# Optimization experiments

Hardware: AMD Instinct MI355X
Metric: run time of the kernel (lower is better)

Reference implementation:

```python
import jax, jax.numpy as jnp
import numpy as np

N = 50000      # number of atoms/nodes
D = 32         # atom_dim == units (pad_length = 0)
E = 300000     # number of bonds/edges
BD = 16        # bond_dim
STEPS = 4      # message passing steps


def setup_inputs() -> dict:
    key = jax.random.key(0)
    ks = jax.random.split(key, 8)
    atom_features = jax.random.normal(ks[0], (N, D), dtype=jnp.float32)
    bond_features = jax.random.uniform(ks[1], (E, BD), dtype=jnp.float32)
    pair_indices = jax.random.randint(ks[2], (E, 2), 0, N, dtype=jnp.int32)
    # EdgeNetwork kernel: xavier_uniform on [bond_dim, atom_dim*atom_dim]
    s = float(np.sqrt(6.0 / (BD + D * D)))
    kernel = jax.random.uniform(ks[3], (BD, D * D), dtype=jnp.float32, minval=-s, maxval=s)
    bias = jnp.zeros((D * D,), dtype=jnp.float32)
    # torch.nn.GRUCell init: U(-1/sqrt(H), 1/sqrt(H)), H = D (pad_length = 0)
    stdv = float(1.0 / np.sqrt(D))
    W_ih = jax.random.uniform(ks[4], (3 * D, D), dtype=jnp.float32, minval=-stdv, maxval=stdv)
    W_hh = jax.random.uniform(ks[5], (3 * D, D), dtype=jnp.float32, minval=-stdv, maxval=stdv)
    b_ih = jax.random.uniform(ks[6], (3 * D,), dtype=jnp.float32, minval=-stdv, maxval=stdv)
    b_hh = jax.random.uniform(ks[7], (3 * D,), dtype=jnp.float32, minval=-stdv, maxval=stdv)
    return {
        "atom_features": atom_features,
        "bond_features": bond_features,
        "pair_indices": pair_indices,
        "kernel": kernel,
        "bias": bias,
        "W_ih": W_ih,
        "W_hh": W_hh,
        "b_ih": b_ih,
        "b_hh": b_hh,
    }


def _gru_cell(x, h, W_ih, W_hh, b_ih, b_hh):
    # torch.nn.GRUCell math, gates stacked as (r, z, n)
    gi = x @ W_ih.T + b_ih  # [N, 3D]
    gh = h @ W_hh.T + b_hh  # [N, 3D]
    i_r, i_z, i_n = jnp.split(gi, 3, axis=-1)
    h_r, h_z, h_n = jnp.split(gh, 3, axis=-1)
    r = jax.nn.sigmoid(i_r + h_r)
    z = jax.nn.sigmoid(i_z + h_z)
    n = jnp.tanh(i_n + r * h_n)
    return (1.0 - z) * n + z * h


def reference(atom_features, bond_features, pair_indices, kernel, bias, W_ih, W_hh, b_ih, b_hh):
    # pad_length = units - atom_dim = 0, so no padding needed.
    W = kernel.reshape(BD, D, D)   # per-bond-feature DxD transforms
    Bm = bias.reshape(D, D)        # bias as DxD matrix applied to neighbor feats
    dst = pair_indices[:, 0]       # aggregation (index_add) target
    src = pair_indices[:, 1]       # gathered neighbor

    h = atom_features
    for _ in range(STEPS):
        nbr = h[src]  # [E, D] gather
        # transformed[e, i] = sum_j (bond[e] @ kernel + bias)[i, j] * nbr[e, j]
        msg = jnp.einsum('eb,bij,ej->ei', bond_features, W, nbr) + nbr @ Bm.T
        agg = jax.ops.segment_sum(msg, dst, num_segments=N)  # scatter-add
        h = _gru_cell(agg, h, W_ih, W_hh, b_ih, b_hh)
    return h
```

## Files before the change

### kernel.cpp

```cpp
#include <hip/hip_runtime.h>
#include <math.h>

#define N_ATOMS 50000
#define D 32
#define E_EDGES 300000
#define BD 16
#define SW 544
#define SCAN_BLOCKS ((N_ATOMS + 255) / 256)
#define GRU_TILE 8
#define GRU_NT (N_ATOMS / GRU_TILE)

#define NB 32
#define FBLOCKS ((N_ATOMS + NB - 1) / NB)

__device__ __forceinline__ float sigmoidf_(float x) {
    return 1.0f / (1.0f + __expf(-x));
}


__global__ void k_build_wt(const float* __restrict__ kern,
                           const float* __restrict__ bias,
                           float* __restrict__ WTj) {
    int idx = blockIdx.x * 256 + threadIdx.x;
    if (idx >= 32 * SW) return;
    int j = idx / SW;
    int r = idx - j * SW;
    int b = r >> 5, i = r & 31;
    WTj[idx] = (b < BD) ? kern[b * 1024 + i * 32 + j] : bias[i * 32 + j];
}

__global__ void k_hist(const int* __restrict__ pair, int* __restrict__ deg, int col) {
    int e = blockIdx.x * 256 + threadIdx.x;
    if (e < E_EDGES) atomicAdd(&deg[pair[2 * e + col]], 1);
}

__global__ void k_scan1(const int* __restrict__ deg, int* __restrict__ offs,
                        int* __restrict__ bsums) {
    __shared__ int sm[256];
    int t = threadIdx.x, gid = blockIdx.x * 256 + t;
    int v = (gid < N_ATOMS) ? deg[gid] : 0;
    sm[t] = v;
    __syncthreads();
    for (int off = 1; off < 256; off <<= 1) {
        int x = (t >= off) ? sm[t - off] : 0;
        __syncthreads();
        sm[t] += x;
        __syncthreads();
    }
    if (gid < N_ATOMS) offs[gid] = sm[t] - v;
    if (t == 255) bsums[blockIdx.x] = sm[255];
}

__global__ void k_scan2(const int* __restrict__ bsums, int* __restrict__ boffs, int nb) {
    __shared__ int sm[256];
    int t = threadIdx.x;
    int v = (t < nb) ? bsums[t] : 0;
    sm[t] = v;
    __syncthreads();
    for (int off = 1; off < 256; off <<= 1) {
        int x = (t >= off) ? sm[t - off] : 0;
        __syncthreads();
        sm[t] += x;
        __syncthreads();
    }
    if (t < nb) boffs[t] = sm[t] - v;
}

__global__ void k_scan3(int* __restrict__ offs, const int* __restrict__ boffs) {
    int gid = blockIdx.x * 256 + threadIdx.x;
    if (gid < N_ATOMS) offs[gid] += boffs[blockIdx.x];
}

__global__ void k_scatter_perm(const int* __restrict__ pair, const int* __restrict__ offs,
                               int* __restrict__ cursor, const float* __restrict__ bond,
                               float* __restrict__ bond_perm, int* __restrict__ dstid) {
    int e = blockIdx.x * 256 + threadIdx.x;
    if (e >= E_EDGES) return;
    int d = pair[2 * e], s = pair[2 * e + 1];
    int pos = offs[s] + atomicAdd(&cursor[s], 1);
    dstid[pos] = d;
    const float4* src4 = (const float4*)(bond + (size_t)e * BD);
    float4* dst4 = (float4*)(bond_perm + (size_t)pos * BD);
    dst4[0] = src4[0];
    dst4[1] = src4[1];
    dst4[2] = src4[2];
    dst4[3] = src4[3];
}

__global__ void k_dstpos(const int* __restrict__ dstid, const int* __restrict__ offs2,
                         int* __restrict__ cursor2, int* __restrict__ wpos) {
    int p = blockIdx.x * 256 + threadIdx.x;
    if (p >= E_EDGES) return;
    int d = dstid[p];
    wpos[p] = offs2[d] + atomicAdd(&cursor2[d], 1);
}

#define EDGE_FMA(M, B0, B1, B2, B3, YN) do {            \
    M = fmaf(B0.x, YN[0],  M); M = fmaf(B0.y, YN[1],  M); \
    M = fmaf(B0.z, YN[2],  M); M = fmaf(B0.w, YN[3],  M); \
    M = fmaf(B1.x, YN[4],  M); M = fmaf(B1.y, YN[5],  M); \
    M = fmaf(B1.z, YN[6],  M); M = fmaf(B1.w, YN[7],  M); \
    M = fmaf(B2.x, YN[8],  M); M = fmaf(B2.y, YN[9],  M); \
    M = fmaf(B2.z, YN[10], M); M = fmaf(B2.w, YN[11], M); \
    M = fmaf(B3.x, YN[12], M); M = fmaf(B3.y, YN[13], M); \
    M = fmaf(B3.z, YN[14], M); M = fmaf(B3.w, YN[15], M); \
} while (0)

__global__ __launch_bounds__(256, 2)
void k_msg(const float* __restrict__ h_in, float* __restrict__ msg_d,
           const float* __restrict__ bond_perm, const int* __restrict__ wpos,
           const float* __restrict__ WTj,
           const int* __restrict__ offs, const int* __restrict__ deg) {
    __shared__ float h_lds[NB][33];

    const int t = threadIdx.x;
    const int bbase = blockIdx.x * NB;
    const int i = t & 31;
    const int grp = t >> 5;
    const int hn0 = grp * 4;

#pragma unroll
    for (int k = 0; k < 4; ++k) {
        const int idx = t + 256 * k;
        const int n = idx >> 5, j = idx & 31;
        const int node = bbase + n;
        h_lds[n][j] = (node < N_ATOMS) ? h_in[(size_t)node * D + j] : 0.f;
    }

    int stv[4], env[4];
#pragma unroll
    for (int n = 0; n < 4; ++n) {
        const int node = bbase + hn0 + n;
        const bool ok = (node < N_ATOMS);
        const int o = ok ? offs[node] : 0;
        stv[n] = o;
        env[n] = o + (ok ? deg[node] : 0);
    }
    __syncthreads();

    float y[4][17];
#pragma unroll
    for (int n = 0; n < 4; ++n)
#pragma unroll
        for (int b = 0; b < 17; ++b) y[n][b] = 0.f;

    for (int j = 0; j < 32; ++j) {
        float wv[17];
#pragma unroll
        for (int b = 0; b < 17; ++b)
            wv[b] = WTj[j * SW + b * 32 + i];
#pragma unroll
        for (int n = 0; n < 4; ++n) {
            const float hv = h_lds[hn0 + n][j];
#pragma unroll
            for (int b = 0; b < 17; ++b)
                y[n][b] = fmaf(wv[b], hv, y[n][b]);
        }
    }

#pragma unroll
    for (int n = 0; n < 4; ++n) {
        int p = stv[n];
        const int e = env[n];
        for (; p + 2 <= e; p += 2) {
            const float4* bp0 = (const float4*)(bond_perm + (size_t)p * BD);
            const float4* bp1 = (const float4*)(bond_perm + (size_t)(p + 1) * BD);
            const int w0 = wpos[p];
            const int w1 = wpos[p + 1];
            const float4 a0 = bp0[0], a1 = bp0[1], a2 = bp0[2], a3 = bp0[3];
            const float4 c0 = bp1[0], c1 = bp1[1], c2 = bp1[2], c3 = bp1[3];
            float m0 = y[n][16];
            float m1 = y[n][16];
            EDGE_FMA(m0, a0, a1, a2, a3, y[n]);
            EDGE_FMA(m1, c0, c1, c2, c3, y[n]);
            msg_d[(size_t)w0 * D + i] = m0;
            msg_d[(size_t)w1 * D + i] = m1;
        }
        if (p < e) {
            const float4* bp0 = (const float4*)(bond_perm + (size_t)p * BD);
            const int w0 = wpos[p];
            const float4 a0 = bp0[0], a1 = bp0[1], a2 = bp0[2], a3 = bp0[3];
            float m0 = y[n][16];
            EDGE_FMA(m0, a0, a1, a2, a3, y[n]);
            msg_d[(size_t)w0 * D + i] = m0;
        }
    }
}

__global__ __launch_bounds__(256, 2)
void k_aggru(const float* __restrict__ msg_d,
             const int* __restrict__ offs2, const int* __restrict__ deg2,
             const float* __restrict__ h_in, float* __restrict__ h_out,
             const float* __restrict__ Wih, const float* __restrict__ Whh,
             const float* __restrict__ bih, const float* __restrict__ bhh) {
    __shared__ float Wih_s[96][33];
    __shared__ float Whh_s[96][33];
    __shared__ float bih_s[96], bhh_s[96];
    __shared__ float x_lds[GRU_TILE][32];
    __shared__ float h_lds[GRU_TILE][32];

    const int t = threadIdx.x;

    for (int idx = t; idx < 96 * 32; idx += 256) {
        const int o = idx >> 5, jj = idx & 31;
        Wih_s[o][jj] = Wih[idx];
        Whh_s[o][jj] = Whh[idx];
    }
    if (t < 96) { bih_s[t] = bih[t]; bhh_s[t] = bhh[t]; }

    const int r = t >> 5;
    const int i = t & 31;
    const int stride = gridDim.x;

    for (int tile = blockIdx.x; tile < GRU_NT; tile += stride) {
        const int node = tile * GRU_TILE + r;
        const int st = offs2[node];
        const int en = st + deg2[node];
        float acc = 0.f;
        int p = st;
        for (; p + 4 <= en; p += 4) {
            const float a0 = msg_d[(size_t)(p + 0) * D + i];
            const float a1 = msg_d[(size_t)(p + 1) * D + i];
            const float a2 = msg_d[(size_t)(p + 2) * D + i];
            const float a3 = msg_d[(size_t)(p + 3) * D + i];
            acc += (a0 + a1) + (a2 + a3);
        }
        for (; p < en; ++p) acc += msg_d[(size_t)p * D + i];
        x_lds[r][i] = acc;
        ((float*)h_lds)[t] = h_in[tile * 256 + t];
        __syncthreads();

        float gri = bih_s[i],      grh = bhh_s[i];
        float gzi = bih_s[32 + i], gzh = bhh_s[32 + i];
        float gni = bih_s[64 + i], gnh = bhh_s[64 + i];
#pragma unroll 8
        for (int jj = 0; jj < 32; ++jj) {
            const float xv = x_lds[r][jj];
            const float hv = h_lds[r][jj];
            gri = fmaf(Wih_s[i][jj],      xv, gri);
            gzi = fmaf(Wih_s[32 + i][jj], xv, gzi);
            gni = fmaf(Wih_s[64 + i][jj], xv, gni);
            grh = fmaf(Whh_s[i][jj],      hv, grh);
            gzh = fmaf(Whh_s[32 + i][jj], hv, gzh);
            gnh = fmaf(Whh_s[64 + i][jj], hv, gnh);
        }
        const float rg = sigmoidf_(gri + grh);
        const float zg = sigmoidf_(gzi + gzh);
        float xn = gni + rg * gnh;
        xn = fminf(fmaxf(xn, -15.f), 15.f);
        const float e2 = __expf(2.f * xn);
        const float ng = (e2 - 1.f) / (e2 + 1.f);
        h_out[tile * 256 + t] = (1.f - zg) * ng + zg * h_lds[r][i];
        __syncthreads();
    }
}

extern "C" void kernel_launch(void* const* d_in, const int* in_sizes, int n_in,
                              void* d_out, int out_size, void* d_ws, size_t ws_size,
                              hipStream_t stream) {
    const float* atom = (const float*)d_in[0];
    const float* bond = (const float*)d_in[1];
    const int*   pair = (const int*)d_in[2];
    const float* kern = (const float*)d_in[3];
    const float* bias = (const float*)d_in[4];
    const float* Wih  = (const float*)d_in[5];
    const float* Whh  = (const float*)d_in[6];
    const float* bih  = (const float*)d_in[7];
    const float* bhh  = (const float*)d_in[8];
    float* out = (float*)d_out;

    char* w = (char*)d_ws;
    auto alloc = [&](size_t bytes) {
        char* p = w;
        w += (bytes + 255) & ~size_t(255);
        return p;
    };
    float* hA        = (float*)alloc((size_t)N_ATOMS * D * 4);
    float* WTj       = (float*)alloc((size_t)32 * SW * 4);
    int*   deg       = (int*)alloc((size_t)N_ATOMS * 4);
    int*   offs      = (int*)alloc((size_t)N_ATOMS * 4);
    int*   deg2      = (int*)alloc((size_t)N_ATOMS * 4);
    int*   offs2     = (int*)alloc((size_t)N_ATOMS * 4);
    int*   cursor    = (int*)alloc((size_t)N_ATOMS * 4);
    int*   cursor2   = (int*)alloc((size_t)N_ATOMS * 4);
    int*   bsums     = (int*)alloc(256 * 4);
    int*   boffs     = (int*)alloc(256 * 4);
    int*   dstid     = (int*)alloc((size_t)E_EDGES * 4);
    int*   wpos      = (int*)alloc((size_t)E_EDGES * 4);
    float* bond_perm = (float*)alloc((size_t)E_EDGES * BD * 4);
    float* msg_d     = (float*)alloc((size_t)E_EDGES * D * 4);

    hipMemsetAsync(deg, 0, (size_t)N_ATOMS * 4, stream);
    hipMemsetAsync(deg2, 0, (size_t)N_ATOMS * 4, stream);
    hipMemsetAsync(cursor, 0, (size_t)N_ATOMS * 4, stream);
    hipMemsetAsync(cursor2, 0, (size_t)N_ATOMS * 4, stream);

    k_build_wt<<<(32 * SW + 255) / 256, 256, 0, stream>>>(kern, bias, WTj);
    k_hist<<<(E_EDGES + 255) / 256, 256, 0, stream>>>(pair, deg, 1);
    k_scan1<<<SCAN_BLOCKS, 256, 0, stream>>>(deg, offs, bsums);
    k_scan2<<<1, 256, 0, stream>>>(bsums, boffs, SCAN_BLOCKS);
    k_scan3<<<SCAN_BLOCKS, 256, 0, stream>>>(offs, boffs);
    k_hist<<<(E_EDGES + 255) / 256, 256, 0, stream>>>(pair, deg2, 0);
    k_scan1<<<SCAN_BLOCKS, 256, 0, stream>>>(deg2, offs2, bsums);
    k_scan2<<<1, 256, 0, stream>>>(bsums, boffs, SCAN_BLOCKS);
    k_scan3<<<SCAN_BLOCKS, 256, 0, stream>>>(offs2, boffs);
    k_scatter_perm<<<(E_EDGES + 255) / 256, 256, 0, stream>>>(pair, offs, cursor,
                                                              bond, bond_perm, dstid);
    k_dstpos<<<(E_EDGES + 255) / 256, 256, 0, stream>>>(dstid, offs2, cursor2, wpos);

    const float* hsrc = atom;
    float* hdst[4] = { hA, out, hA, out };
    for (int s = 0; s < 4; ++s) {
        k_msg<<<FBLOCKS, 256, 0, stream>>>(hsrc, msg_d, bond_perm, wpos,
                                           WTj, offs, deg);
        k_aggru<<<2048, 256, 0, stream>>>(msg_d, offs2, deg2, hsrc, hdst[s],
                                          Wih, Whh, bih, bhh);
        hsrc = hdst[s];
    }
}
```

Baseline: 564.2 us.

## Write messages contiguously in source order and gather them by index in aggregation

The message kernel now writes each edge's message at its source-sorted position instead of scattering it to the destination-sorted slot. The aggregation kernel reads it back through a new reverse-position index. This turns scattered writes into coalesced ones at the cost of indirect gathered reads plus an extra index load per edge. The message kernel also doubles its nodes per block from 32 to 64 (8 per warp group). That reuses each weight load across more nodes but raises register pressure, since y grows to 8x17 floats.

```diff
diff --git a/kernel.cpp b/kernel.cpp
--- a/kernel.cpp
+++ b/kernel.cpp
@@ -10,7 +10,7 @@
 #define GRU_TILE 8
 #define GRU_NT (N_ATOMS / GRU_TILE)
 
-#define NB 32
+#define NB 64
 #define FBLOCKS ((N_ATOMS + NB - 1) / NB)
 
 __device__ __forceinline__ float sigmoidf_(float x) {
@@ -87,12 +87,13 @@
     dst4[3] = src4[3];
 }
 
-__global__ void k_dstpos(const int* __restrict__ dstid, const int* __restrict__ offs2,
-                         int* __restrict__ cursor2, int* __restrict__ wpos) {
+__global__ void k_rpos(const int* __restrict__ dstid, const int* __restrict__ offs2,
+                       int* __restrict__ cursor2, int* __restrict__ rpos) {
     int p = blockIdx.x * 256 + threadIdx.x;
     if (p >= E_EDGES) return;
     int d = dstid[p];
-    wpos[p] = offs2[d] + atomicAdd(&cursor2[d], 1);
+    int slot = offs2[d] + atomicAdd(&cursor2[d], 1);
+    rpos[slot] = p;
 }
 
 #define EDGE_FMA(M, B0, B1, B2, B3, YN) do {            \
@@ -108,8 +109,7 @@
 
 __global__ __launch_bounds__(256, 2)
 void k_msg(const float* __restrict__ h_in, float* __restrict__ msg_d,
-           const float* __restrict__ bond_perm, const int* __restrict__ wpos,
-           const float* __restrict__ WTj,
+           const float* __restrict__ bond_perm, const float* __restrict__ WTj,
            const int* __restrict__ offs, const int* __restrict__ deg) {
     __shared__ float h_lds[NB][33];
 
@@ -117,19 +117,19 @@
     const int bbase = blockIdx.x * NB;
     const int i = t & 31;
     const int grp = t >> 5;
-    const int hn0 = grp * 4;
-
-#pragma unroll
-    for (int k = 0; k < 4; ++k) {
+    const int hn0 = grp * 8;
+
+#pragma unroll
+    for (int k = 0; k < 8; ++k) {
         const int idx = t + 256 * k;
         const int n = idx >> 5, j = idx & 31;
         const int node = bbase + n;
         h_lds[n][j] = (node < N_ATOMS) ? h_in[(size_t)node * D + j] : 0.f;
     }
 
-    int stv[4], env[4];
-#pragma unroll
-    for (int n = 0; n < 4; ++n) {
+    int stv[8], env[8];
+#pragma unroll
+    for (int n = 0; n < 8; ++n) {
         const int node = bbase + hn0 + n;
         const bool ok = (node < N_ATOMS);
         const int o = ok ? offs[node] : 0;
@@ -138,9 +138,9 @@
     }
     __syncthreads();
 
-    float y[4][17];
-#pragma unroll
-    for (int n = 0; n < 4; ++n)
+    float y[8][17];
+#pragma unroll
+    for (int n = 0; n < 8; ++n)
 #pragma unroll
         for (int b = 0; b < 17; ++b) y[n][b] = 0.f;
 
@@ -150,7 +150,7 @@
         for (int b = 0; b < 17; ++b)
             wv[b] = WTj[j * SW + b * 32 + i];
 #pragma unroll
-        for (int n = 0; n < 4; ++n) {
+        for (int n = 0; n < 8; ++n) {
             const float hv = h_lds[hn0 + n][j];
 #pragma unroll
             for (int b = 0; b < 17; ++b)
@@ -159,36 +159,33 @@
     }
 
 #pragma unroll
-    for (int n = 0; n < 4; ++n) {
+    for (int n = 0; n < 8; ++n) {
         int p = stv[n];
         const int e = env[n];
         for (; p + 2 <= e; p += 2) {
             const float4* bp0 = (const float4*)(bond_perm + (size_t)p * BD);
             const float4* bp1 = (const float4*)(bond_perm + (size_t)(p + 1) * BD);
-            const int w0 = wpos[p];
-            const int w1 = wpos[p + 1];
             const float4 a0 = bp0[0], a1 = bp0[1], a2 = bp0[2], a3 = bp0[3];
             const float4 c0 = bp1[0], c1 = bp1[1], c2 = bp1[2], c3 = bp1[3];
             float m0 = y[n][16];
             float m1 = y[n][16];
             EDGE_FMA(m0, a0, a1, a2, a3, y[n]);
             EDGE_FMA(m1, c0, c1, c2, c3, y[n]);
-            msg_d[(size_t)w0 * D + i] = m0;
-            msg_d[(size_t)w1 * D + i] = m1;
+            msg_d[(size_t)p * D + i] = m0;
+            msg_d[(size_t)(p + 1) * D + i] = m1;
         }
         if (p < e) {
             const float4* bp0 = (const float4*)(bond_perm + (size_t)p * BD);
-            const int w0 = wpos[p];
             const float4 a0 = bp0[0], a1 = bp0[1], a2 = bp0[2], a3 = bp0[3];
             float m0 = y[n][16];
             EDGE_FMA(m0, a0, a1, a2, a3, y[n]);
-            msg_d[(size_t)w0 * D + i] = m0;
+            msg_d[(size_t)p * D + i] = m0;
         }
     }
 }
 
 __global__ __launch_bounds__(256, 2)
-void k_aggru(const float* __restrict__ msg_d,
+void k_aggru(const float* __restrict__ msg_d, const int* __restrict__ rpos,
              const int* __restrict__ offs2, const int* __restrict__ deg2,
              const float* __restrict__ h_in, float* __restrict__ h_out,
              const float* __restrict__ Wih, const float* __restrict__ Whh,
@@ -219,13 +216,18 @@
         float acc = 0.f;
         int p = st;
         for (; p + 4 <= en; p += 4) {
-            const float a0 = msg_d[(size_t)(p + 0) * D + i];
-            const float a1 = msg_d[(size_t)(p + 1) * D + i];
-            const float a2 = msg_d[(size_t)(p + 2) * D + i];
-            const float a3 = msg_d[(size_t)(p + 3) * D + i];
+            const int p0 = rpos[p + 0];
+            const int p1 = rpos[p + 1];
+            const int p2 = rpos[p + 2];
+            const int p3 = rpos[p + 3];
+            const float a0 = msg_d[(size_t)p0 * D + i];
+            const float a1 = msg_d[(size_t)p1 * D + i];
+            const float a2 = msg_d[(size_t)p2 * D + i];
+            const float a3 = msg_d[(size_t)p3 * D + i];
             acc += (a0 + a1) + (a2 + a3);
         }
-        for (; p < en; ++p) acc += msg_d[(size_t)p * D + i];
+        for (; p < en; ++p)
+            acc += msg_d[(size_t)rpos[p] * D + i];
         x_lds[r][i] = acc;
         ((float*)h_lds)[t] = h_in[tile * 256 + t];
         __syncthreads();
@@ -286,7 +288,7 @@
     int*   bsums     = (int*)alloc(256 * 4);
     int*   boffs     = (int*)alloc(256 * 4);
     int*   dstid     = (int*)alloc((size_t)E_EDGES * 4);
-    int*   wpos      = (int*)alloc((size_t)E_EDGES * 4);
+    int*   rpos      = (int*)alloc((size_t)E_EDGES * 4);
     float* bond_perm = (float*)alloc((size_t)E_EDGES * BD * 4);
     float* msg_d     = (float*)alloc((size_t)E_EDGES * D * 4);
 
@@ -306,14 +308,13 @@
     k_scan3<<<SCAN_BLOCKS, 256, 0, stream>>>(offs2, boffs);
     k_scatter_perm<<<(E_EDGES + 255) / 256, 256, 0, stream>>>(pair, offs, cursor,
                                                               bond, bond_perm, dstid);
-    k_dstpos<<<(E_EDGES + 255) / 256, 256, 0, stream>>>(dstid, offs2, cursor2, wpos);
+    k_rpos<<<(E_EDGES + 255) / 256, 256, 0, stream>>>(dstid, offs2, cursor2, rpos);
 
     const float* hsrc = atom;
     float* hdst[4] = { hA, out, hA, out };
     for (int s = 0; s < 4; ++s) {
-        k_msg<<<FBLOCKS, 256, 0, stream>>>(hsrc, msg_d, bond_perm, wpos,
-                                           WTj, offs, deg);
-        k_aggru<<<2048, 256, 0, stream>>>(msg_d, offs2, deg2, hsrc, hdst[s],
+        k_msg<<<FBLOCKS, 256, 0, stream>>>(hsrc, msg_d, bond_perm, WTj, offs, deg);
+        k_aggru<<<2048, 256, 0, stream>>>(msg_d, rpos, offs2, deg2, hsrc, hdst[s],
                                           Wih, Whh, bih, bhh);
         hsrc = hdst[s];
     }
```

Result: slower. 584.9 us (+3.7%).
